# Kernel optimization log

Hardware: AMD Instinct MI355X
Metric: run time of the kernel (lower is better)

Reference implementation:

```python
import jax, jax.numpy as jnp
import numpy as np

N, W, MAX_DEPTH = 250_000, 784, 16
N_NODES = 2 ** MAX_DEPTH + 1  # 65537
DEPTH = MAX_DEPTH - 1  # deepest traversal that keeps indices in-range


def setup_inputs() -> dict:
    key = jax.random.key(0)
    k1, k2, k3 = jax.random.split(key, 3)
    x = jax.random.randint(k1, (N, W), 0, 2, dtype=jnp.int32)  # binary features
    node_choices = jax.random.randint(k2, (N_NODES,), 0, W, dtype=jnp.int32)
    node_predictions = jax.random.randint(k3, (N_NODES,), 0, 2).astype(jnp.float32)
    return {"x": x, "node_choices": node_choices,
            "node_predictions": node_predictions, "depth": DEPTH}


def reference(x, node_choices, node_predictions, depth):
    # Sequential decision-tree traversal: at each level gather the split
    # feature index for every sample's current node, read that feature bit,
    # and descend to child 2*n+1 (bit=0) or 2*n+2 (bit=1).
    n = x.shape[0]
    nodes0 = jnp.zeros((n,), dtype=jnp.int32)

    def body(_, nodes):
        choices = node_choices[nodes]                                   # [n]
        decisions = jnp.take_along_axis(x, choices[:, None].astype(jnp.int32), axis=1)[:, 0]
        return nodes * 2 + decisions + 1

    nodes = jax.lax.fori_loop(0, depth, body, nodes0)
    return node_predictions[nodes].astype(jnp.bool_)
```

## Files before the change

### kernel.cpp

```cpp
#include <hip/hip_runtime.h>
#include <hip/hip_bf16.h>

__global__ __launch_bounds__(256) void Tree_17867063951635_kernel(
    const int* __restrict__ x,
    const int* __restrict__ choices,
    const float* __restrict__ preds,
    const int* __restrict__ depth_p,
    int* __restrict__ out,
    int n, int w)
{
    const int i = blockIdx.x * blockDim.x + threadIdx.x;
    if (i >= n) return;

    const int depth = *depth_p;
    const int* __restrict__ row = x + (long long)i * (long long)w;

    int node = 0;
    for (int d = 0; d < depth; ++d) {
        const int c   = choices[node];
        const int bit = row[c];
        node = node * 2 + bit + 1;
    }
    out[i] = (preds[node] != 0.0f) ? 1 : 0;
}

extern "C" void kernel_launch(void* const* d_in, const int* in_sizes, int n_in,
                              void* d_out, int out_size, void* d_ws, size_t ws_size,
                              hipStream_t stream) {
    const int*   x       = (const int*)d_in[0];
    const int*   choices = (const int*)d_in[1];
    const float* preds   = (const float*)d_in[2];
    const int*   depth_p = (const int*)d_in[3];
    int*         out     = (int*)d_out;

    const int n = out_size;
    const int w = in_sizes[0] / n;

    const int block = 256;
    const int grid  = (n + block - 1) / block;
    Tree_17867063951635_kernel<<<grid, block, 0, stream>>>(
        x, choices, preds, depth_p, out, n, w);
}
```

Measured before the change: 910.9 us.

## Stream rows coalesced into LDS bitmasks before traversing the tree

Each block now reads its 256 rows of x with fully coalesced wave-wide loads and packs every row into 32-bit bitmasks in LDS using ballot. The 15-level traversal then reads feature bits from LDS instead of doing dependent scattered global gathers. This replaces latency-bound random accesses with one sequential pass over all of x, so it reads far more bytes in total. A template specialization for w=784 fixes the segment counts at compile time.

```diff
diff --git a/kernel.cpp b/kernel.cpp
--- a/kernel.cpp
+++ b/kernel.cpp
@@ -1,27 +1,58 @@
 #include <hip/hip_runtime.h>
-#include <hip/hip_bf16.h>
 
+
+template <int NSEG_C, int TAIL_C>
 __global__ __launch_bounds__(256) void Tree_17867063951635_kernel(
-    const int* __restrict__ x,
-    const int* __restrict__ choices,
+    const int*   __restrict__ x,
+    const int*   __restrict__ choices,
     const float* __restrict__ preds,
-    const int* __restrict__ depth_p,
-    int* __restrict__ out,
+    const int*   __restrict__ depth_p,
+    int*         __restrict__ out,
     int n, int w)
 {
-    const int i = blockIdx.x * blockDim.x + threadIdx.x;
-    if (i >= n) return;
+    extern __shared__ unsigned lds[];
 
-    const int depth = *depth_p;
-    const int* __restrict__ row = x + (long long)i * (long long)w;
+    const int tid  = threadIdx.x;
+    const int lane = tid & 63;
+    const int wid  = tid >> 6;
+    const long long blockRow0 = (long long)blockIdx.x * 256;
 
-    int node = 0;
-    for (int d = 0; d < depth; ++d) {
-        const int c   = choices[node];
-        const int bit = row[c];
-        node = node * 2 + bit + 1;
+    const int nseg = NSEG_C ? NSEG_C : (w >> 6);
+    const int tail = NSEG_C ? TAIL_C : (w & 63);
+
+    for (int rr = 0; rr < 64; ++rr) {
+        const int r = (wid << 6) + rr;
+        const long long grow = blockRow0 + r;
+        if (grow < n) {
+            const int* __restrict__ rowp = x + grow * (long long)w;
+            #pragma unroll
+            for (int seg = 0; seg < nseg; ++seg) {
+                const int v = rowp[(seg << 6) + lane];
+                const unsigned long long m = __ballot(v != 0);
+                if (lane < 2)
+                    lds[((seg << 1) + lane) * 256 + r] = (unsigned)(m >> (lane << 5));
+            }
+            if (tail) {
+                const int v = (lane < tail) ? rowp[(nseg << 6) + lane] : 0;
+                const unsigned long long m = __ballot(v != 0);
+                if (lane < 2 && (lane << 5) < tail)
+                    lds[((nseg << 1) + lane) * 256 + r] = (unsigned)(m >> (lane << 5));
+            }
+        }
     }
-    out[i] = (preds[node] != 0.0f) ? 1 : 0;
+    __syncthreads();
+
+    const long long i = blockRow0 + tid;
+    if (i < n) {
+        const int depth = *depth_p;
+        int node = 0;
+        for (int d = 0; d < depth; ++d) {
+            const int c = choices[node];
+            const unsigned bits = lds[(c >> 5) * 256 + tid];
+            node = (node << 1) + (int)((bits >> (c & 31)) & 1u) + 1;
+        }
+        out[i] = (preds[node] != 0.0f) ? 1 : 0;
+    }
 }
 
 extern "C" void kernel_launch(void* const* d_in, const int* in_sizes, int n_in,
@@ -38,6 +69,14 @@
 
     const int block = 256;
     const int grid  = (n + block - 1) / block;
-    Tree_17867063951635_kernel<<<grid, block, 0, stream>>>(
-        x, choices, preds, depth_p, out, n, w);
+    const int wpr   = (w + 31) / 32;
+    const size_t lds_bytes = (size_t)wpr * 256 * sizeof(unsigned);
+
+    if (w == 784) {
+        Tree_17867063951635_kernel<12, 16><<<grid, block, lds_bytes, stream>>>(
+            x, choices, preds, depth_p, out, n, w);
+    } else {
+        Tree_17867063951635_kernel<0, 0><<<grid, block, lds_bytes, stream>>>(
+            x, choices, preds, depth_p, out, n, w);
+    }
 }
```

New measurement: 1.235 ms. 1.36x slower.

## Bit-pack binary features in a streaming pass before the tree traversal

Applied to the files above, without the earlier changes.

Adds a pack kernel that streams each int32 feature row and compresses it into bitmasks using wave ballots, writing 25 words per row into the workspace. The traversal kernel then gathers single bits from this much smaller packed array, replacing scattered 4-byte loads from the full 784 MB input. The aim is to swap latency-bound random gathers over a huge array for one coalesced streaming read plus cache-friendly lookups. The cost is an extra full pass over the input and an extra kernel launch. If the workspace is too small, the code falls back to the original direct kernel.

```diff
diff --git a/kernel.cpp b/kernel.cpp
--- a/kernel.cpp
+++ b/kernel.cpp
@@ -1,20 +1,78 @@
 #include <hip/hip_runtime.h>
-#include <hip/hip_bf16.h>
 
-__global__ __launch_bounds__(256) void Tree_17867063951635_kernel(
+
+template <int NSEG_C, int TAIL_C>
+__global__ __launch_bounds__(256) void pack_kernel(
     const int* __restrict__ x,
-    const int* __restrict__ choices,
+    unsigned*  __restrict__ packed,
+    int n, int w, int nseg_rt, int tail_rt, int wpr)
+{
+    const int  gtid = blockIdx.x * blockDim.x + threadIdx.x;
+    const int  wave = gtid >> 6;
+    const int  lane = gtid & 63;
+    const long long row0 = (long long)wave * 4;
+
+    const int nseg = NSEG_C ? NSEG_C : nseg_rt;
+    const int tail = NSEG_C ? TAIL_C : tail_rt;
+
+    #pragma unroll
+    for (int rr = 0; rr < 4; ++rr) {
+        const long long r = row0 + rr;
+        if (r >= n) return;
+        const int* __restrict__ rowp = x + r * (long long)w;
+        unsigned*  __restrict__ outp = packed + r * (long long)wpr;
+
+        #pragma unroll
+        for (int seg = 0; seg < nseg; ++seg) {
+            const int v = rowp[(seg << 6) + lane];
+            const unsigned long long m = __ballot(v != 0);
+            if (lane < 2)
+                outp[(seg << 1) + lane] = (unsigned)(m >> (lane << 5));
+        }
+        if (tail) {
+            const int v = (lane < tail) ? rowp[(nseg << 6) + lane] : 0;
+            const unsigned long long m = __ballot(v != 0);
+            if (lane < 2 && (lane << 5) < tail)
+                outp[(nseg << 1) + lane] = (unsigned)(m >> (lane << 5));
+        }
+    }
+}
+
+__global__ __launch_bounds__(256) void traverse_kernel(
+    const unsigned* __restrict__ packed,
+    const int*      __restrict__ choices,
+    const float*    __restrict__ preds,
+    const int*      __restrict__ depth_p,
+    int*            __restrict__ out,
+    int n, int wpr)
+{
+    const int i = blockIdx.x * blockDim.x + threadIdx.x;
+    if (i >= n) return;
+
+    const unsigned* __restrict__ row = packed + (long long)i * wpr;
+    const int depth = *depth_p;
+
+    int node = 0;
+    for (int d = 0; d < depth; ++d) {
+        const int c = choices[node];
+        const unsigned bits = row[c >> 5];
+        node = (node << 1) + (int)((bits >> (c & 31)) & 1u) + 1;
+    }
+    out[i] = (preds[node] != 0.0f) ? 1 : 0;
+}
+
+__global__ __launch_bounds__(256) void direct_kernel(
+    const int*   __restrict__ x,
+    const int*   __restrict__ choices,
     const float* __restrict__ preds,
-    const int* __restrict__ depth_p,
-    int* __restrict__ out,
+    const int*   __restrict__ depth_p,
+    int*         __restrict__ out,
     int n, int w)
 {
     const int i = blockIdx.x * blockDim.x + threadIdx.x;
     if (i >= n) return;
-
     const int depth = *depth_p;
     const int* __restrict__ row = x + (long long)i * (long long)w;
-
     int node = 0;
     for (int d = 0; d < depth; ++d) {
         const int c   = choices[node];
@@ -36,8 +94,36 @@
     const int n = out_size;
     const int w = in_sizes[0] / n;
 
-    const int block = 256;
-    const int grid  = (n + block - 1) / block;
-    Tree_17867063951635_kernel<<<grid, block, 0, stream>>>(
-        x, choices, preds, depth_p, out, n, w);
+    const int wpr = (w + 31) / 32;
+    const size_t need = (size_t)n * wpr * sizeof(unsigned);
+
+    if (ws_size < need) {
+        const int block = 256;
+        const int grid  = (n + block - 1) / block;
+        direct_kernel<<<grid, block, 0, stream>>>(x, choices, preds, depth_p,
+                                                  out, n, w);
+        return;
+    }
+
+    unsigned* packed = (unsigned*)d_ws;
+
+    {
+        const int block = 256;
+        const long long waves = ((long long)n + 3) / 4;
+        const long long grid  = (waves + 3) / 4;
+        const int nseg = w >> 6, tail = w & 63;
+        if (w == 784)
+            pack_kernel<12, 16><<<dim3((unsigned)grid), block, 0, stream>>>(
+                x, packed, n, w, nseg, tail, wpr);
+        else
+            pack_kernel<0, 0><<<dim3((unsigned)grid), block, 0, stream>>>(
+                x, packed, n, w, nseg, tail, wpr);
+    }
+
+    {
+        const int block = 256;
+        const int grid  = (n + block - 1) / block;
+        traverse_kernel<<<grid, block, 0, stream>>>(packed, choices, preds,
+                                                    depth_p, out, n, wpr);
+    }
 }
```

Measured after the change: 1.077 ms. 1.18x slower.

## Bit-pack feature rows into workspace then traverse tree from shared memory

Applied to the files above, without the earlier changes.

Adds a pack kernel that streams each 784-int binary row and compresses it into 25 32-bit words in the workspace, laid out transposed per 256-row block. A second kernel loads a block's packed bits into LDS and does all 15 traversal steps from shared memory. This replaces 15 dependent, latency-bound random global gathers per sample with one sequential pass over x. The cost is an extra kernel launch and a workspace round trip. The pack loads are strided per thread, so each row is read contiguously by one thread rather than coalesced across lanes.

```diff
diff --git a/kernel.cpp b/kernel.cpp
--- a/kernel.cpp
+++ b/kernel.cpp
@@ -1,20 +1,93 @@
 #include <hip/hip_runtime.h>
-#include <hip/hip_bf16.h>
 
-__global__ __launch_bounds__(256) void Tree_17867063951635_kernel(
+
+#define WPR 25
+
+__global__ __launch_bounds__(256) void pack_kernel(
     const int* __restrict__ x,
-    const int* __restrict__ choices,
+    unsigned*  __restrict__ packed,
+    int n)
+{
+    const int tid = threadIdx.x;
+    const long long r = (long long)blockIdx.x * 256 + tid;
+    if (r >= n) return;
+
+    const int4* __restrict__ rowp = (const int4*)(x + r * 784LL);
+    unsigned acc[WPR];
+
+    #pragma unroll 2
+    for (int ww = 0; ww < 24; ++ww) {
+        unsigned a = 0;
+        #pragma unroll
+        for (int j = 0; j < 8; ++j) {
+            const int4 v = rowp[(ww << 3) + j];
+            a |= (unsigned)(v.x & 1) << ((j << 2) + 0);
+            a |= (unsigned)(v.y & 1) << ((j << 2) + 1);
+            a |= (unsigned)(v.z & 1) << ((j << 2) + 2);
+            a |= (unsigned)(v.w & 1) << ((j << 2) + 3);
+        }
+        acc[ww] = a;
+    }
+    {
+        unsigned a = 0;
+        #pragma unroll
+        for (int j = 0; j < 4; ++j) {
+            const int4 v = rowp[192 + j];
+            a |= (unsigned)(v.x & 1) << ((j << 2) + 0);
+            a |= (unsigned)(v.y & 1) << ((j << 2) + 1);
+            a |= (unsigned)(v.z & 1) << ((j << 2) + 2);
+            a |= (unsigned)(v.w & 1) << ((j << 2) + 3);
+        }
+        acc[24] = a;
+    }
+
+    unsigned* __restrict__ outp = packed + (long long)blockIdx.x * (WPR * 256);
+    #pragma unroll
+    for (int ww = 0; ww < WPR; ++ww)
+        outp[ww * 256 + tid] = acc[ww];
+}
+
+__global__ __launch_bounds__(256) void traverse_kernel(
+    const unsigned* __restrict__ packed,
+    const int*      __restrict__ choices,
+    const float*    __restrict__ preds,
+    const int*      __restrict__ depth_p,
+    int* __restrict__ out, int n)
+{
+    __shared__ unsigned bits[WPR * 256];
+
+    const int tid = threadIdx.x;
+    const unsigned* __restrict__ src = packed + (long long)blockIdx.x * (WPR * 256);
+    #pragma unroll
+    for (int k = 0; k < WPR; ++k)
+        bits[k * 256 + tid] = src[k * 256 + tid];
+    __syncthreads();
+
+    const long long i = (long long)blockIdx.x * 256 + tid;
+    if (i >= n) return;
+
+    const int depth = *depth_p;
+    int node = 0;
+    for (int d = 0; d < depth; ++d) {
+        const int c = choices[node];
+        const unsigned wv = bits[(c >> 5) * 256 + tid];
+        node = (node << 1) + (int)((wv >> (c & 31)) & 1u) + 1;
+    }
+    out[i] = (preds[node] != 0.0f) ? 1 : 0;
+}
+
+__global__ __launch_bounds__(256) void direct_kernel(
+    const int*   __restrict__ x,
+    const int*   __restrict__ choices,
     const float* __restrict__ preds,
-    const int* __restrict__ depth_p,
-    int* __restrict__ out,
+    const int*   __restrict__ depth_p,
+    int*         __restrict__ out,
     int n, int w)
 {
     const int i = blockIdx.x * blockDim.x + threadIdx.x;
     if (i >= n) return;
-
     const int depth = *depth_p;
     const int* __restrict__ row = x + (long long)i * (long long)w;
-
     int node = 0;
     for (int d = 0; d < depth; ++d) {
         const int c   = choices[node];
@@ -36,8 +109,20 @@
     const int n = out_size;
     const int w = in_sizes[0] / n;
 
-    const int block = 256;
-    const int grid  = (n + block - 1) / block;
-    Tree_17867063951635_kernel<<<grid, block, 0, stream>>>(
-        x, choices, preds, depth_p, out, n, w);
+    const long long nblk = (n + 255) / 256;
+    const size_t need = (size_t)nblk * WPR * 256 * sizeof(unsigned);
+
+    if (w != 784 || ws_size < need) {
+        const int block = 256;
+        const int grid  = (n + block - 1) / block;
+        direct_kernel<<<grid, block, 0, stream>>>(x, choices, preds, depth_p,
+                                                  out, n, w);
+        return;
+    }
+
+    unsigned* packed = (unsigned*)d_ws;
+
+    pack_kernel<<<dim3((unsigned)nblk), 256, 0, stream>>>(x, packed, n);
+    traverse_kernel<<<dim3((unsigned)nblk), 256, 0, stream>>>(
+        packed, choices, preds, depth_p, out, n);
 }
```

After: 1.041 ms. 1.14x slower.
